# Optimization experiments

Measured on AMD Instinct MI355X. Metric: run time of the kernel, lower is better.

## Reference

```python
import jax, jax.numpy as jnp
import numpy as np

B, S, D, H, E, K = 4, 2048, 1024, 2048, 8, 2
TEMP = 5.0
EPS = 1e-9


def setup_inputs() -> dict:
    key = jax.random.key(0)
    k_x, k_wg, k_w1, k_w2 = jax.random.split(key, 4)
    scale = 0.02
    return {
        "x": jax.random.normal(k_x, (B, S, D), dtype=jnp.float32),
        "Wg": jax.random.normal(k_wg, (D, E), dtype=jnp.float32) * scale,
        "bg": jnp.zeros((E,), dtype=jnp.float32),
        "W1": jax.random.normal(k_w1, (E, D, H), dtype=jnp.float32) * scale,
        "b1": jnp.zeros((E, H), dtype=jnp.float32),
        "W2": jax.random.normal(k_w2, (E, H, D), dtype=jnp.float32) * scale,
        "b2": jnp.zeros((E, D), dtype=jnp.float32),
    }


def reference(x, Wg, bg, W1, b1, W2, b2):
    # Gating: softmax over experts with temperature
    logits = jnp.einsum('bsd,de->bse', x, Wg) + bg  # [B,S,E]
    probs = jax.nn.softmax(logits / TEMP, axis=-1)
    # Top-k mask, renormalized (zeros for non-selected experts)
    vals, idx = jax.lax.top_k(probs, K)              # [B,S,K]
    onehot = jax.nn.one_hot(idx, E, dtype=x.dtype)   # [B,S,K,E]
    mask = jnp.einsum('bske,bsk->bse', onehot, vals) # scatter topk values
    gates = mask / (jnp.sum(mask, axis=-1, keepdims=True) + EPS)
    # Expert FFNs (dense over experts; gate weight is exactly 0 for unrouted)
    h = jax.nn.gelu(jnp.einsum('bsd,edh->besh', x, W1) + b1[None, :, None, :],
                    approximate=False)               # [B,E,S,H]
    out = jnp.einsum('besh,ehd->besd', h, W2) + b2[None, :, None, :]
    y = jnp.einsum('bse,besd->bsd', gates, out)      # weighted combine
    return y
```

## Files before the change

kernel.cpp:

```cpp
#include <hip/hip_runtime.h>
#include <stdint.h>

#define NTOK 8192
#define DIM  1024
#define HID  2048
#define NE   8
#define CAP  17408
#define TM 128
#define TN 128
#define TKK 64

typedef __bf16  bf16x8  __attribute__((ext_vector_type(8)));
typedef float   floatx4 __attribute__((ext_vector_type(4)));

__device__ __forceinline__ unsigned short f2bf(float f) {
  union { float f; unsigned u; } v; v.f = f;
  unsigned r = v.u + 0x7FFFu + ((v.u >> 16) & 1u);
  return (unsigned short)(r >> 16);
}

__device__ __forceinline__ void async_ld16(const unsigned short* g, unsigned short* l) {
  __builtin_amdgcn_global_load_lds(
      (const __attribute__((address_space(1))) unsigned int*)(const void*)g,
      (__attribute__((address_space(3))) unsigned int*)(void*)l, 16, 0, 0);
}

__global__ void transpose_cast_kernel(const float* __restrict__ src,
                                      unsigned short* __restrict__ dst,
                                      int R, int C) {
  __shared__ unsigned short T[64][65];
  int e = blockIdx.z;
  const float* S = src + (size_t)e * R * C;
  unsigned short* D2 = dst + (size_t)e * R * C;
  int c0 = blockIdx.x * 64;
  int r0 = blockIdx.y * 64;
  int col = threadIdx.x & 63;
  int rr  = threadIdx.x >> 6;
#pragma unroll
  for (int i = 0; i < 16; i++) {
    int r = rr + i * 4;
    T[col][r] = f2bf(S[(size_t)(r0 + r) * C + c0 + col]);
  }
  __syncthreads();
#pragma unroll
  for (int i = 0; i < 16; i++) {
    int r = rr + i * 4;
    D2[(size_t)(c0 + r) * R + r0 + col] = T[r][col];
  }
}

__global__ __launch_bounds__(256)
void gating_kernel(const float* __restrict__ x, const float* __restrict__ Wg,
                   const float* __restrict__ bg, int* __restrict__ tok_e,
                   float* __restrict__ tok_g, unsigned short* __restrict__ xb) {
  __shared__ float WgS[NE * DIM];
  int tid = threadIdx.x;
#pragma unroll
  for (int j = 0; j < NE * DIM / 256; j++) {
    int i = j * 256 + tid;
    WgS[(i & 7) * DIM + (i >> 3)] = Wg[i];
  }
  __syncthreads();
  int wave = tid >> 6;
  int lane = tid & 63;
#pragma unroll
  for (int ti = 0; ti < 2; ti++) {
    int t = blockIdx.x * 8 + wave * 2 + ti;
    const float* xr = x + (size_t)t * DIM;
    float p[NE];
#pragma unroll
    for (int e = 0; e < NE; e++) p[e] = 0.f;
#pragma unroll
    for (int it = 0; it < DIM / 256; it++) {
      int d = (it * 64 + lane) * 4;
      float4 xv = *(const float4*)&xr[d];
      uint2 o;
      o.x = (unsigned)f2bf(xv.x) | ((unsigned)f2bf(xv.y) << 16);
      o.y = (unsigned)f2bf(xv.z) | ((unsigned)f2bf(xv.w) << 16);
      *(uint2*)&xb[(size_t)t * DIM + d] = o;
#pragma unroll
      for (int e = 0; e < NE; e++) {
        float4 wv = *(const float4*)&WgS[e * DIM + d];
        p[e] += xv.x * wv.x + xv.y * wv.y + xv.z * wv.z + xv.w * wv.w;
      }
    }
#pragma unroll
    for (int e = 0; e < NE; e++) {
#pragma unroll
      for (int off = 32; off > 0; off >>= 1) p[e] += __shfl_xor(p[e], off);
    }
    if (lane == 0) {
      float s[NE];
      float m = -1e30f;
#pragma unroll
      for (int e = 0; e < NE; e++) { s[e] = (p[e] + bg[e]) * 0.2f; m = fmaxf(m, s[e]); }
      float sum = 0.f;
#pragma unroll
      for (int e = 0; e < NE; e++) { s[e] = expf(s[e] - m); sum += s[e]; }
      float inv = 1.0f / sum;
      int i0 = 0; float v0 = -1.f;
#pragma unroll
      for (int e = 0; e < NE; e++) { float pe = s[e] * inv; if (pe > v0) { v0 = pe; i0 = e; } }
      int i1 = -1; float v1 = -1.f;
#pragma unroll
      for (int e = 0; e < NE; e++) {
        if (e == i0) continue;
        float pe = s[e] * inv; if (pe > v1) { v1 = pe; i1 = e; }
      }
      float den = v0 + v1 + 1e-9f;
      tok_e[t * 2]     = i0; tok_g[t * 2]     = v0 / den;
      tok_e[t * 2 + 1] = i1; tok_g[t * 2 + 1] = v1 / den;
    }
  }
}

__global__ __launch_bounds__(256)
void count_kernel(const int* __restrict__ tok_e, int* __restrict__ cnt) {
  __shared__ int hist[NE];
  int tid = threadIdx.x;
  if (tid < NE) hist[tid] = 0;
  __syncthreads();
  int i0 = blockIdx.x * 512 + tid;
  atomicAdd(&hist[tok_e[i0]], 1);
  atomicAdd(&hist[tok_e[i0 + 256]], 1);
  __syncthreads();
  if (tid < NE) atomicAdd(&cnt[tid], hist[tid]);
}

__global__ void offsets_kernel(const int* __restrict__ cnt, int* __restrict__ seg) {
  if (threadIdx.x == 0 && blockIdx.x == 0) {
    int s = 0;
    for (int e = 0; e < NE; e++) { seg[e] = s; s += ((cnt[e] + TM - 1) / TM) * TM; }
    seg[NE] = s;
  }
}

__global__ __launch_bounds__(256)
void route_kernel(const int* __restrict__ tok_e, const float* __restrict__ tok_g,
                  const int* __restrict__ seg, int* __restrict__ cnt2,
                  int* __restrict__ token_row, float* __restrict__ gate_row,
                  int* __restrict__ tok_pos) {
  __shared__ int hist[NE];
  __shared__ int base[NE];
  int tid = threadIdx.x;
  if (tid < NE) hist[tid] = 0;
  __syncthreads();
  int t = blockIdx.x * 256 + tid;
  int e0 = tok_e[t * 2];
  int e1 = tok_e[t * 2 + 1];
  int r0 = atomicAdd(&hist[e0], 1);
  int r1 = atomicAdd(&hist[e1], 1);
  __syncthreads();
  if (tid < NE) base[tid] = atomicAdd(&cnt2[tid], hist[tid]);
  __syncthreads();
  int p0 = seg[e0] + base[e0] + r0;
  int p1 = seg[e1] + base[e1] + r1;
  token_row[p0] = t; gate_row[p0] = tok_g[t * 2];     tok_pos[t * 2]     = p0;
  token_row[p1] = t; gate_row[p1] = tok_g[t * 2 + 1]; tok_pos[t * 2 + 1] = p1;
}

__global__ __launch_bounds__(256)
void gemm1_kernel(const unsigned short* __restrict__ xb, const unsigned short* __restrict__ w1t,
                  const float* __restrict__ b1, const int* __restrict__ token_row,
                  const int* __restrict__ seg, const unsigned short* __restrict__ zbuf,
                  unsigned short* __restrict__ hbuf) {
  __shared__ __align__(16) unsigned short As[TM * TKK];
  __shared__ __align__(16) unsigned short Bs[TN * TKK];
  int row0 = blockIdx.y * TM;
  int total = seg[NE];
  if (row0 >= total) return;
  int e = 0;
  while (row0 >= seg[e + 1]) e++;
  int n0 = blockIdx.x * TN;
  int tid = threadIdx.x;
  int lane = tid & 63;
  int w = tid >> 6;
  int wm = tid >> 7;
  int wn = (tid >> 6) & 1;
  int lrow = lane >> 3;
  int lk   = (lane & 7) * 8;

  floatx4 zero4 = {0.f, 0.f, 0.f, 0.f};
  floatx4 acc[4][4];
#pragma unroll
  for (int a = 0; a < 4; a++)
#pragma unroll
    for (int b = 0; b < 4; b++) acc[a][b] = zero4;

  const unsigned short* w1e = w1t + (size_t)e * DIM * HID;
  const unsigned short* srcA[4];
  const unsigned short* srcB[4];
#pragma unroll
  for (int i = 0; i < 4; i++) {
    int r = w * 32 + i * 8 + lrow;
    int t = token_row[row0 + r];
    srcA[i] = (t >= 0 ? xb + (size_t)t * DIM : zbuf) + lk;
    srcB[i] = w1e + (size_t)(n0 + r) * DIM + lk;
  }

  int mr = lane & 15;
  int kq = (lane >> 4) * 8;

  for (int k0 = 0; k0 < DIM; k0 += TKK) {
#pragma unroll
    for (int i = 0; i < 4; i++) {
      async_ld16(srcA[i] + k0, &As[(w * 32 + i * 8 + lrow) * TKK + lk]);
      async_ld16(srcB[i] + k0, &Bs[(w * 32 + i * 8 + lrow) * TKK + lk]);
    }
    __syncthreads();
#pragma unroll
    for (int kk = 0; kk < TKK; kk += 32) {
      bf16x8 af[4], bfr[4];
#pragma unroll
      for (int im = 0; im < 4; im++)
        af[im] = *(const bf16x8*)&As[(wm * 64 + im * 16 + mr) * TKK + kk + kq];
#pragma unroll
      for (int in = 0; in < 4; in++)
        bfr[in] = *(const bf16x8*)&Bs[(wn * 64 + in * 16 + mr) * TKK + kk + kq];
#pragma unroll
      for (int im = 0; im < 4; im++)
#pragma unroll
        for (int in = 0; in < 4; in++)
          acc[im][in] = __builtin_amdgcn_mfma_f32_16x16x32_bf16(af[im], bfr[in], acc[im][in], 0, 0, 0);
    }
    __syncthreads();
  }
  int quad = lane >> 4;
  int c16 = lane & 15;
  const float* b1e = b1 + e * HID;
#pragma unroll
  for (int im = 0; im < 4; im++) {
    int rb = row0 + wm * 64 + im * 16 + quad * 4;
#pragma unroll
    for (int in = 0; in < 4; in++) {
      int c = n0 + wn * 64 + in * 16 + c16;
      float bias = b1e[c];
#pragma unroll
      for (int i = 0; i < 4; i++) {
        float v = acc[im][in][i] + bias;
        v = 0.5f * v * (1.0f + erff(v * 0.70710678118654752f));
        hbuf[(size_t)(rb + i) * HID + c] = f2bf(v);
      }
    }
  }
}

__global__ __launch_bounds__(256)
void gemm2_kernel(const unsigned short* __restrict__ hbuf, const unsigned short* __restrict__ w2t,
                  const float* __restrict__ b2, const float* __restrict__ gate_row,
                  const int* __restrict__ seg, unsigned short* __restrict__ obuf) {
  __shared__ __align__(16) unsigned short As[TM * TKK];
  __shared__ __align__(16) unsigned short Bs[TN * TKK];
  int row0 = blockIdx.y * TM;
  int total = seg[NE];
  if (row0 >= total) return;
  int e = 0;
  while (row0 >= seg[e + 1]) e++;
  int n0 = blockIdx.x * TN;
  int tid = threadIdx.x;
  int lane = tid & 63;
  int w = tid >> 6;
  int wm = tid >> 7;
  int wn = (tid >> 6) & 1;
  int lrow = lane >> 3;
  int lk   = (lane & 7) * 8;

  floatx4 zero4 = {0.f, 0.f, 0.f, 0.f};
  floatx4 acc[4][4];
#pragma unroll
  for (int a = 0; a < 4; a++)
#pragma unroll
    for (int b = 0; b < 4; b++) acc[a][b] = zero4;

  const unsigned short* w2e = w2t + (size_t)e * DIM * HID;
  const unsigned short* srcA[4];
  const unsigned short* srcB[4];
#pragma unroll
  for (int i = 0; i < 4; i++) {
    int r = w * 32 + i * 8 + lrow;
    srcA[i] = hbuf + (size_t)(row0 + r) * HID + lk;
    srcB[i] = w2e + (size_t)(n0 + r) * HID + lk;
  }

  int mr = lane & 15;
  int kq = (lane >> 4) * 8;

  for (int k0 = 0; k0 < HID; k0 += TKK) {
#pragma unroll
    for (int i = 0; i < 4; i++) {
      async_ld16(srcA[i] + k0, &As[(w * 32 + i * 8 + lrow) * TKK + lk]);
      async_ld16(srcB[i] + k0, &Bs[(w * 32 + i * 8 + lrow) * TKK + lk]);
    }
    __syncthreads();
#pragma unroll
    for (int kk = 0; kk < TKK; kk += 32) {
      bf16x8 af[4], bfr[4];
#pragma unroll
      for (int im = 0; im < 4; im++)
        af[im] = *(const bf16x8*)&As[(wm * 64 + im * 16 + mr) * TKK + kk + kq];
#pragma unroll
      for (int in = 0; in < 4; in++)
        bfr[in] = *(const bf16x8*)&Bs[(wn * 64 + in * 16 + mr) * TKK + kk + kq];
#pragma unroll
      for (int im = 0; im < 4; im++)
#pragma unroll
        for (int in = 0; in < 4; in++)
          acc[im][in] = __builtin_amdgcn_mfma_f32_16x16x32_bf16(af[im], bfr[in], acc[im][in], 0, 0, 0);
    }
    __syncthreads();
  }
  int quad = lane >> 4;
  int c16 = lane & 15;
  const float* b2e = b2 + e * DIM;
#pragma unroll
  for (int im = 0; im < 4; im++) {
    int rb = row0 + wm * 64 + im * 16 + quad * 4;
    float gs[4];
#pragma unroll
    for (int i = 0; i < 4; i++) gs[i] = gate_row[rb + i];
#pragma unroll
    for (int in = 0; in < 4; in++) {
      int c = n0 + wn * 64 + in * 16 + c16;
      float bias = b2e[c];
#pragma unroll
      for (int i = 0; i < 4; i++) {
        float val = gs[i] * (acc[im][in][i] + bias);
        obuf[(size_t)(rb + i) * DIM + c] = f2bf(val);
      }
    }
  }
}

__global__ void combine_kernel(const unsigned short* __restrict__ obuf,
                               const int* __restrict__ tok_pos,
                               float* __restrict__ y) {
  int idx = blockIdx.x * 256 + threadIdx.x;
  int t = idx >> 7;
  int c = (idx & 127) << 3;
  int p0 = tok_pos[t * 2];
  int p1 = tok_pos[t * 2 + 1];
  uint4 a = *(const uint4*)(obuf + (size_t)p0 * DIM + c);
  uint4 b = *(const uint4*)(obuf + (size_t)p1 * DIM + c);
  float out[8];
  unsigned au[4] = {a.x, a.y, a.z, a.w};
  unsigned bu[4] = {b.x, b.y, b.z, b.w};
#pragma unroll
  for (int i = 0; i < 4; i++) {
    union { unsigned u; float f; } lo0, hi0, lo1, hi1;
    lo0.u = au[i] << 16; hi0.u = au[i] & 0xFFFF0000u;
    lo1.u = bu[i] << 16; hi1.u = bu[i] & 0xFFFF0000u;
    out[i * 2]     = lo0.f + lo1.f;
    out[i * 2 + 1] = hi0.f + hi1.f;
  }
  float* yp = y + (size_t)t * DIM + c;
  *(float4*)yp       = *(float4*)&out[0];
  *(float4*)(yp + 4) = *(float4*)&out[4];
}

extern "C" void kernel_launch(void* const* d_in, const int* in_sizes, int n_in,
                              void* d_out, int out_size, void* d_ws, size_t ws_size,
                              hipStream_t stream) {
  const float* x  = (const float*)d_in[0];
  const float* Wg = (const float*)d_in[1];
  const float* bg = (const float*)d_in[2];
  const float* W1 = (const float*)d_in[3];
  const float* b1 = (const float*)d_in[4];
  const float* W2 = (const float*)d_in[5];
  const float* b2 = (const float*)d_in[6];
  float* y = (float*)d_out;
  char* ws = (char*)d_ws;

  constexpr size_t OFF_META = 0;
  constexpr size_t OFF_TOKE = 256;
  constexpr size_t OFF_TOKG = OFF_TOKE + (size_t)NTOK * 2 * 4;
  constexpr size_t OFF_TPOS = OFF_TOKG + (size_t)NTOK * 2 * 4;
  constexpr size_t OFF_TROW = OFF_TPOS + (size_t)NTOK * 2 * 4;
  constexpr size_t OFF_GROW = OFF_TROW + (size_t)CAP * 4;
  constexpr size_t OFF_ZB   = OFF_GROW + (size_t)CAP * 4;
  constexpr size_t OFF_XB   = OFF_ZB  + (size_t)DIM * 2;
  constexpr size_t OFF_W1T  = OFF_XB  + (size_t)NTOK * DIM * 2;
  constexpr size_t OFF_W2T  = OFF_W1T + (size_t)NE * DIM * HID * 2;
  constexpr size_t OFF_H    = OFF_W2T + (size_t)NE * DIM * HID * 2;
  constexpr size_t OFF_OBUF = OFF_XB;

  int* cnt        = (int*)(ws + OFF_META);
  int* cnt2       = (int*)(ws + OFF_META + 64);
  int* seg        = (int*)(ws + OFF_META + 128);
  int* tok_e      = (int*)(ws + OFF_TOKE);
  float* tok_g    = (float*)(ws + OFF_TOKG);
  int* tok_pos    = (int*)(ws + OFF_TPOS);
  int* token_row  = (int*)(ws + OFF_TROW);
  float* gate_row = (float*)(ws + OFF_GROW);
  unsigned short* zbuf = (unsigned short*)(ws + OFF_ZB);
  unsigned short* xb   = (unsigned short*)(ws + OFF_XB);
  unsigned short* w1t  = (unsigned short*)(ws + OFF_W1T);
  unsigned short* w2t  = (unsigned short*)(ws + OFF_W2T);
  unsigned short* hbuf = (unsigned short*)(ws + OFF_H);
  unsigned short* obuf = (unsigned short*)(ws + OFF_OBUF);

  hipMemsetAsync(ws, 0, 192, stream);
  hipMemsetAsync(token_row, 0xFF, (size_t)CAP * 4, stream);
  hipMemsetAsync(zbuf, 0, (size_t)DIM * 2, stream);

  transpose_cast_kernel<<<dim3(HID / 64, DIM / 64, NE), 256, 0, stream>>>(W1, w1t, DIM, HID);
  transpose_cast_kernel<<<dim3(DIM / 64, HID / 64, NE), 256, 0, stream>>>(W2, w2t, HID, DIM);
  gating_kernel<<<NTOK / 8, 256, 0, stream>>>(x, Wg, bg, tok_e, tok_g, xb);
  count_kernel<<<NTOK * 2 / 512, 256, 0, stream>>>(tok_e, cnt);
  offsets_kernel<<<1, 64, 0, stream>>>(cnt, seg);
  route_kernel<<<NTOK / 256, 256, 0, stream>>>(tok_e, tok_g, seg, cnt2, token_row, gate_row, tok_pos);
  gemm1_kernel<<<dim3(HID / TN, CAP / TM), 256, 0, stream>>>(xb, w1t, b1, token_row, seg, zbuf, hbuf);
  gemm2_kernel<<<dim3(DIM / TN, CAP / TM), 256, 0, stream>>>(hbuf, w2t, b2, gate_row, seg, obuf);
  combine_kernel<<<NTOK * DIM / 8 / 256, 256, 0, stream>>>(obuf, tok_pos, y);
}
```

Measured before the change: 499.9 us.

## Merge weight transposes, swap MFMA operands for vector epilogue stores, use tanh GELU

```diff
diff --git a/kernel.cpp b/kernel.cpp
--- a/kernel.cpp
+++ b/kernel.cpp
@@ -25,15 +25,34 @@
       (__attribute__((address_space(3))) unsigned int*)(void*)l, 16, 0, 0);
 }
 
-__global__ void transpose_cast_kernel(const float* __restrict__ src,
-                                      unsigned short* __restrict__ dst,
-                                      int R, int C) {
+__device__ __forceinline__ float gelu_fast(float v) {
+  float g = 0.79788456080286536f * (v + 0.044715f * v * v * v);
+  float t = __builtin_amdgcn_exp2f(-2.8853900817779268f * g);
+  return v * __builtin_amdgcn_rcpf(1.0f + t);
+}
+
+__device__ __forceinline__ uint2 pack4bf(float a, float b, float c, float d) {
+  uint2 o;
+  o.x = (unsigned)f2bf(a) | ((unsigned)f2bf(b) << 16);
+  o.y = (unsigned)f2bf(c) | ((unsigned)f2bf(d) << 16);
+  return o;
+}
+
+__global__ void transpose_cast_kernel(const float* __restrict__ W1, const float* __restrict__ W2,
+                                      unsigned short* __restrict__ w1t, unsigned short* __restrict__ w2t) {
   __shared__ unsigned short T[64][65];
-  int e = blockIdx.z;
-  const float* S = src + (size_t)e * R * C;
-  unsigned short* D2 = dst + (size_t)e * R * C;
-  int c0 = blockIdx.x * 64;
-  int r0 = blockIdx.y * 64;
+  int z = blockIdx.z;
+  const float* S;
+  unsigned short* D2;
+  int R, C, c0, r0;
+  if (z < NE) {
+    S = W1 + (size_t)z * DIM * HID; D2 = w1t + (size_t)z * DIM * HID;
+    R = DIM; C = HID; c0 = blockIdx.x * 64; r0 = blockIdx.y * 64;
+  } else {
+    int e = z - NE;
+    S = W2 + (size_t)e * HID * DIM; D2 = w2t + (size_t)e * HID * DIM;
+    R = HID; C = DIM; c0 = blockIdx.y * 64; r0 = blockIdx.x * 64;
+  }
   int col = threadIdx.x & 63;
   int rr  = threadIdx.x >> 6;
 #pragma unroll
@@ -74,10 +93,7 @@
     for (int it = 0; it < DIM / 256; it++) {
       int d = (it * 64 + lane) * 4;
       float4 xv = *(const float4*)&xr[d];
-      uint2 o;
-      o.x = (unsigned)f2bf(xv.x) | ((unsigned)f2bf(xv.y) << 16);
-      o.y = (unsigned)f2bf(xv.z) | ((unsigned)f2bf(xv.w) << 16);
-      *(uint2*)&xb[(size_t)t * DIM + d] = o;
+      *(uint2*)&xb[(size_t)t * DIM + d] = pack4bf(xv.x, xv.y, xv.z, xv.w);
 #pragma unroll
       for (int e = 0; e < NE; e++) {
         float4 wv = *(const float4*)&WgS[e * DIM + d];
@@ -174,11 +190,10 @@
   int n0 = blockIdx.x * TN;
   int tid = threadIdx.x;
   int lane = tid & 63;
-  int w = tid >> 6;
   int wm = tid >> 7;
   int wn = (tid >> 6) & 1;
-  int lrow = lane >> 3;
-  int lk   = (lane & 7) * 8;
+  int rbase = tid >> 3;
+  int colseg = (tid & 7) * 8;
 
   floatx4 zero4 = {0.f, 0.f, 0.f, 0.f};
   floatx4 acc[4][4];
@@ -192,10 +207,10 @@
   const unsigned short* srcB[4];
 #pragma unroll
   for (int i = 0; i < 4; i++) {
-    int r = w * 32 + i * 8 + lrow;
+    int r = rbase + i * 32;
     int t = token_row[row0 + r];
-    srcA[i] = (t >= 0 ? xb + (size_t)t * DIM : zbuf) + lk;
-    srcB[i] = w1e + (size_t)(n0 + r) * DIM + lk;
+    srcA[i] = (t >= 0 ? xb + (size_t)t * DIM : zbuf) + colseg;
+    srcB[i] = w1e + (size_t)(n0 + r) * DIM + colseg;
   }
 
   int mr = lane & 15;
@@ -204,8 +219,8 @@
   for (int k0 = 0; k0 < DIM; k0 += TKK) {
 #pragma unroll
     for (int i = 0; i < 4; i++) {
-      async_ld16(srcA[i] + k0, &As[(w * 32 + i * 8 + lrow) * TKK + lk]);
-      async_ld16(srcB[i] + k0, &Bs[(w * 32 + i * 8 + lrow) * TKK + lk]);
+      async_ld16(srcA[i] + k0, &As[(rbase + i * 32) * TKK + colseg]);
+      async_ld16(srcB[i] + k0, &Bs[(rbase + i * 32) * TKK + colseg]);
     }
     __syncthreads();
 #pragma unroll
@@ -221,7 +236,7 @@
       for (int im = 0; im < 4; im++)
 #pragma unroll
         for (int in = 0; in < 4; in++)
-          acc[im][in] = __builtin_amdgcn_mfma_f32_16x16x32_bf16(af[im], bfr[in], acc[im][in], 0, 0, 0);
+          acc[im][in] = __builtin_amdgcn_mfma_f32_16x16x32_bf16(bfr[in], af[im], acc[im][in], 0, 0, 0);
     }
     __syncthreads();
   }
@@ -230,17 +245,16 @@
   const float* b1e = b1 + e * HID;
 #pragma unroll
   for (int im = 0; im < 4; im++) {
-    int rb = row0 + wm * 64 + im * 16 + quad * 4;
+    int r = row0 + wm * 64 + im * 16 + c16;
 #pragma unroll
     for (int in = 0; in < 4; in++) {
-      int c = n0 + wn * 64 + in * 16 + c16;
-      float bias = b1e[c];
-#pragma unroll
-      for (int i = 0; i < 4; i++) {
-        float v = acc[im][in][i] + bias;
-        v = 0.5f * v * (1.0f + erff(v * 0.70710678118654752f));
-        hbuf[(size_t)(rb + i) * HID + c] = f2bf(v);
-      }
+      int c = n0 + wn * 64 + in * 16 + quad * 4;
+      float4 bias = *(const float4*)&b1e[c];
+      float v0 = gelu_fast(acc[im][in][0] + bias.x);
+      float v1 = gelu_fast(acc[im][in][1] + bias.y);
+      float v2 = gelu_fast(acc[im][in][2] + bias.z);
+      float v3 = gelu_fast(acc[im][in][3] + bias.w);
+      *(uint2*)&hbuf[(size_t)r * HID + c] = pack4bf(v0, v1, v2, v3);
     }
   }
 }
@@ -259,11 +273,10 @@
   int n0 = blockIdx.x * TN;
   int tid = threadIdx.x;
   int lane = tid & 63;
-  int w = tid >> 6;
   int wm = tid >> 7;
   int wn = (tid >> 6) & 1;
-  int lrow = lane >> 3;
-  int lk   = (lane & 7) * 8;
+  int rbase = tid >> 3;
+  int colseg = (tid & 7) * 8;
 
   floatx4 zero4 = {0.f, 0.f, 0.f, 0.f};
   floatx4 acc[4][4];
@@ -277,9 +290,9 @@
   const unsigned short* srcB[4];
 #pragma unroll
   for (int i = 0; i < 4; i++) {
-    int r = w * 32 + i * 8 + lrow;
-    srcA[i] = hbuf + (size_t)(row0 + r) * HID + lk;
-    srcB[i] = w2e + (size_t)(n0 + r) * HID + lk;
+    int r = rbase + i * 32;
+    srcA[i] = hbuf + (size_t)(row0 + r) * HID + colseg;
+    srcB[i] = w2e + (size_t)(n0 + r) * HID + colseg;
   }
 
   int mr = lane & 15;
@@ -288,8 +301,8 @@
   for (int k0 = 0; k0 < HID; k0 += TKK) {
 #pragma unroll
     for (int i = 0; i < 4; i++) {
-      async_ld16(srcA[i] + k0, &As[(w * 32 + i * 8 + lrow) * TKK + lk]);
-      async_ld16(srcB[i] + k0, &Bs[(w * 32 + i * 8 + lrow) * TKK + lk]);
+      async_ld16(srcA[i] + k0, &As[(rbase + i * 32) * TKK + colseg]);
+      async_ld16(srcB[i] + k0, &Bs[(rbase + i * 32) * TKK + colseg]);
     }
     __syncthreads();
 #pragma unroll
@@ -305,7 +318,7 @@
       for (int im = 0; im < 4; im++)
 #pragma unroll
         for (int in = 0; in < 4; in++)
-          acc[im][in] = __builtin_amdgcn_mfma_f32_16x16x32_bf16(af[im], bfr[in], acc[im][in], 0, 0, 0);
+          acc[im][in] = __builtin_amdgcn_mfma_f32_16x16x32_bf16(bfr[in], af[im], acc[im][in], 0, 0, 0);
     }
     __syncthreads();
   }
@@ -314,19 +327,17 @@
   const float* b2e = b2 + e * DIM;
 #pragma unroll
   for (int im = 0; im < 4; im++) {
-    int rb = row0 + wm * 64 + im * 16 + quad * 4;
-    float gs[4];
-#pragma unroll
-    for (int i = 0; i < 4; i++) gs[i] = gate_row[rb + i];
+    int r = row0 + wm * 64 + im * 16 + c16;
+    float gs = gate_row[r];
 #pragma unroll
     for (int in = 0; in < 4; in++) {
-      int c = n0 + wn * 64 + in * 16 + c16;
-      float bias = b2e[c];
-#pragma unroll
-      for (int i = 0; i < 4; i++) {
-        float val = gs[i] * (acc[im][in][i] + bias);
-        obuf[(size_t)(rb + i) * DIM + c] = f2bf(val);
-      }
+      int c = n0 + wn * 64 + in * 16 + quad * 4;
+      float4 bias = *(const float4*)&b2e[c];
+      float v0 = gs * (acc[im][in][0] + bias.x);
+      float v1 = gs * (acc[im][in][1] + bias.y);
+      float v2 = gs * (acc[im][in][2] + bias.z);
+      float v3 = gs * (acc[im][in][3] + bias.w);
+      *(uint2*)&obuf[(size_t)r * DIM + c] = pack4bf(v0, v1, v2, v3);
     }
   }
 }
@@ -402,8 +413,7 @@
   hipMemsetAsync(token_row, 0xFF, (size_t)CAP * 4, stream);
   hipMemsetAsync(zbuf, 0, (size_t)DIM * 2, stream);
 
-  transpose_cast_kernel<<<dim3(HID / 64, DIM / 64, NE), 256, 0, stream>>>(W1, w1t, DIM, HID);
-  transpose_cast_kernel<<<dim3(DIM / 64, HID / 64, NE), 256, 0, stream>>>(W2, w2t, HID, DIM);
+  transpose_cast_kernel<<<dim3(32, 16, 16), 256, 0, stream>>>(W1, W2, w1t, w2t);
   gating_kernel<<<NTOK / 8, 256, 0, stream>>>(x, Wg, bg, tok_e, tok_g, xb);
   count_kernel<<<NTOK * 2 / 512, 256, 0, stream>>>(tok_e, cnt);
   offsets_kernel<<<1, 64, 0, stream>>>(cnt, seg);
```

Measured after the change: 484.8 us. 3.0% less time.
